# Kernel tuning notes

Hardware: AMD Instinct MI355X
Metric: run time of the kernel (lower is better)

The kernel has to match this reference:

```python
import jax, jax.numpy as jnp
import numpy as np

B, C_FEAT, C_CODE, H, W = 32, 768, 70, 28, 28
FS = 11
NEG = 5
POS_INTRA_SHIFT = 0.18
POS_INTER_SHIFT = 0.12
NEG_INTER_SHIFT = 0.46


def _norm(t):
    # F.normalize(t, dim=1, eps=1e-10)
    n = jnp.sqrt(jnp.sum(t * t, axis=1, keepdims=True))
    return t / jnp.maximum(n, 1e-10)


def _grid_sample(t, coords):
    # torch: F.grid_sample(t, coords.permute(0,2,1,3), padding_mode='border', align_corners=True)
    grid = jnp.transpose(coords, (0, 2, 1, 3))  # [N, Hg, Wg, 2], last dim = (x, y)
    N, C, Hi, Wi = t.shape
    # align_corners=True unnormalize, then border-clip the continuous coordinate
    x = jnp.clip((grid[..., 0] + 1.0) * 0.5 * (Wi - 1), 0.0, Wi - 1.0)
    y = jnp.clip((grid[..., 1] + 1.0) * 0.5 * (Hi - 1), 0.0, Hi - 1.0)
    x0 = jnp.floor(x)
    y0 = jnp.floor(y)
    wx = (x - x0)[:, None]  # broadcast over channel dim
    wy = (y - y0)[:, None]
    x0i = x0.astype(jnp.int32)
    y0i = y0.astype(jnp.int32)
    x1i = jnp.minimum(x0i + 1, Wi - 1)
    y1i = jnp.minimum(y0i + 1, Hi - 1)
    gather = jax.vmap(lambda img, yi, xi: img[:, yi, xi])  # [C,Hg,Wg] per batch elem
    v00 = gather(t, y0i, x0i)
    v01 = gather(t, y0i, x1i)
    v10 = gather(t, y1i, x0i)
    v11 = gather(t, y1i, x1i)
    return (v00 * (1.0 - wx) * (1.0 - wy) + v01 * wx * (1.0 - wy)
            + v10 * (1.0 - wx) * wy + v11 * wx * wy)


def _helper(f1, f2, c1, c2, shift):
    # fd under torch.no_grad -> stop_gradient
    fd = jnp.einsum('nchw,ncij->nhwij', _norm(f1), _norm(f2))
    old_mean = fd.mean()  # pointwise=True branch
    fd = fd - fd.mean(axis=(3, 4), keepdims=True)
    fd = jax.lax.stop_gradient(fd - fd.mean() + old_mean)
    cd = jnp.einsum('nchw,ncij->nhwij', _norm(c1), _norm(c2))
    # zero_clamp=True -> min_val=0.0; stabalize=True -> clamp max 0.8
    loss = -jnp.clip(cd, 0.0, 0.8) * (fd - shift)
    return loss, cd


def _forward(orig_feats, orig_feats_pos, orig_code, orig_code_pos,
             depth_aug_feats, depth_aug_feats_pos, coords1, coords2, perms):
    c1 = coords1 * 2.0 - 1.0
    c2 = coords2 * 2.0 - 1.0
    feats = _grid_sample(orig_feats, c1)
    code = _grid_sample(orig_code, c1)
    feats_pos = _grid_sample(orig_feats_pos, c2)
    code_pos = _grid_sample(orig_code_pos, c2)
    daf = _grid_sample(depth_aug_feats, c1)
    _ = _grid_sample(depth_aug_feats_pos, c2)  # computed (as in torch) but unused

    pos_intra_loss, pos_intra_cd = _helper(daf, daf, code, code, POS_INTRA_SHIFT)
    pos_inter_loss, pos_inter_cd = _helper(feats, feats_pos, code, code_pos, POS_INTER_SHIFT)

    neg_losses, neg_cds = [], []
    for i in range(perms.shape[0]):  # fixed small neg_samples loop
        p = perms[i]
        feats_neg = _grid_sample(orig_feats[p], c2)
        code_neg = _grid_sample(orig_code[p], c2)
        l, cd = _helper(feats, feats_neg, code, code_neg, NEG_INTER_SHIFT)
        neg_losses.append(l)
        neg_cds.append(cd)
    neg_inter_loss = jnp.concatenate(neg_losses, axis=0)
    neg_inter_cd = jnp.concatenate(neg_cds, axis=0)
    return (pos_intra_loss.mean(), pos_intra_cd,
            pos_inter_loss.mean(), pos_inter_cd,
            neg_inter_loss, neg_inter_cd)


def setup_inputs() -> dict:
    key = jax.random.key(0)
    ks = jax.random.split(key, 10)
    rng = np.random.default_rng(0)
    perms = []
    for _ in range(NEG):  # super_perm: derangement-ish permutation
        p = rng.permutation(B)
        p = np.where(p == np.arange(B), p + 1, p) % B
        perms.append(p)
    return {
        'orig_feats': jax.random.normal(ks[0], (B, C_FEAT, H, W), jnp.float32),
        'orig_feats_pos': jax.random.normal(ks[1], (B, C_FEAT, H, W), jnp.float32),
        'orig_salience': jnp.zeros((B, H, W), jnp.float32),
        'orig_salience_pos': jnp.zeros((B, H, W), jnp.float32),
        'orig_code': jax.random.normal(ks[2], (B, C_CODE, H, W), jnp.float32),
        'orig_code_pos': jax.random.normal(ks[3], (B, C_CODE, H, W), jnp.float32),
        'depth_aug_feats': jax.random.normal(ks[4], (B, C_FEAT, H, W), jnp.float32),
        'depth_aug_feats_pos': jax.random.normal(ks[5], (B, C_FEAT, H, W), jnp.float32),
        'coords1': jax.random.uniform(ks[6], (B, FS, FS, 2), jnp.float32),
        'coords2': jax.random.uniform(ks[7], (B, FS, FS, 2), jnp.float32),
        'perms': jnp.asarray(np.stack(perms), dtype=jnp.int32),
    }


def reference(orig_feats, orig_feats_pos, orig_salience, orig_salience_pos,
              orig_code, orig_code_pos, depth_aug_feats, depth_aug_feats_pos,
              coords1, coords2, perms):
    # use_salience=False: salience tensors unused
    return _forward(orig_feats, orig_feats_pos, orig_code, orig_code_pos,
                    depth_aug_feats, depth_aug_feats_pos, coords1, coords2, perms)
```

## Files before the change

### kernel.cpp

```cpp
#include <hip/hip_runtime.h>

#define CF 768
#define CCODE 70
#define NPIX 784
#define P 121
#define NB 32
#define NTOTF 468512.0f

#define OFF_PI_SCALAR 0
#define OFF_PI_CD 1
#define OFF_PO_SCALAR 468513
#define OFF_PO_CD 468514
#define OFF_NEG_LOSS 937026
#define OFF_NEG_CD 3279586

#define WS_BSUMS 0
#define WS_ADDT 768
#define WS_INVF 1024
#define WS_INVC 33792
#define WS_FRAG_FLOAT 62464
#define FEAT_FRAG_SHORTS 98304
#define CODE_FRAG_SHORTS 12288
#define FEATS_TOTAL_SHORTS (8 * 32 * FEAT_FRAG_SHORTS)
#define CODE_BASE_SHORTS FEATS_TOTAL_SHORTS
#define CODE_TOTAL_SHORTS (7 * 32 * CODE_FRAG_SHORTS)
#define WS_NEED2 (WS_FRAG_FLOAT + (FEATS_TOTAL_SHORTS + CODE_TOTAL_SHORTS) / 2)

typedef __attribute__((ext_vector_type(8))) short short8;
typedef __attribute__((ext_vector_type(4))) float f32x4;
typedef unsigned short ushort_t;
typedef unsigned int uint_t;

__device__ __forceinline__ float samp4(const float* __restrict__ img, int c,
                                       const int4 o, const float4 w) {
  const float* p = img + c * NPIX;
  return w.x * p[o.x] + w.y * p[o.y] + w.z * p[o.z] + w.w * p[o.w];
}

__device__ __forceinline__ void mkcoord(const float* cp, int4* o, float4* w) {
  float x = fminf(fmaxf(cp[0] * 27.f, 0.f), 27.f);
  float y = fminf(fmaxf(cp[1] * 27.f, 0.f), 27.f);
  float x0f = floorf(x), y0f = floorf(y);
  int x0 = (int)x0f, y0 = (int)y0f;
  int x1 = min(x0 + 1, 27), y1 = min(y0 + 1, 27);
  float wx = x - x0f, wy = y - y0f;
  *o = make_int4(y0 * 28 + x0, y0 * 28 + x1, y1 * 28 + x0, y1 * 28 + x1);
  *w = make_float4((1.f - wx) * (1.f - wy), wx * (1.f - wy),
                   (1.f - wx) * wy, wx * wy);
}

__device__ __forceinline__ void mkcoord2(const float* cp, int2* o, float4* w) {
  float x = fminf(fmaxf(cp[0] * 27.f, 0.f), 27.f);
  float y = fminf(fmaxf(cp[1] * 27.f, 0.f), 27.f);
  float x0f = floorf(x), y0f = floorf(y);
  int x0 = (int)x0f, y0 = (int)y0f;
  int y1 = min(y0 + 1, 27);
  float wx = x - x0f, wy = y - y0f;
  bool sh = (x0 >= 27);
  int xb = sh ? 26 : x0;
  float wa0 = sh ? 0.f : (1.f - wx) * (1.f - wy);
  float wa1 = sh ? (1.f - wy) : wx * (1.f - wy);
  float wb0 = sh ? 0.f : (1.f - wx) * wy;
  float wb1 = sh ? wy : wx * wy;
  *o = make_int2(y0 * 28 + xb, y1 * 28 + xb);
  *w = make_float4(wa0, wa1, wb0, wb1);
}

__device__ __forceinline__ ushort_t f2bf(float x) {
  uint_t u = __float_as_uint(x);
  u += 0x7fffu + ((u >> 16) & 1u);
  return (ushort_t)(u >> 16);
}

__device__ __forceinline__ float bflo(uint_t u) {
  return __uint_as_float(u << 16);
}
__device__ __forceinline__ float bfhi(uint_t u) {
  return __uint_as_float(u & 0xffff0000u);
}

__global__ __launch_bounds__(256) void presample_bal(
    const float* __restrict__ OF, const float* __restrict__ OFP,
    const float* __restrict__ OC, const float* __restrict__ OCP,
    const float* __restrict__ DAF,
    const float* __restrict__ CO1, const float* __restrict__ CO2,
    const int* __restrict__ PERMS, float* __restrict__ ws) {
  ushort_t* frags = (ushort_t*)(ws + WS_FRAG_FLOAT);
  __shared__ float planes[8 * NPIX];
  __shared__ int sh_slot[16], sh_n[16], sh_cb[16];
  __shared__ int sh_ncs;
  const int job = (int)(((long long)blockIdx.x * 1013) % 2560);
  const int tid = threadIdx.x;

  int tensor, m, g0, G;
  if (job < 1536) { tensor = 0; m = job / 48; g0 = (job - m * 48) * 2; G = 2; }
  else if (job < 1920) { int j = job - 1536; tensor = 1; m = j / 12; g0 = (j - m * 12) * 8; G = 8; }
  else if (job < 2304) { int j = job - 1920; tensor = 2; m = j / 12; g0 = (j - m * 12) * 8; G = 8; }
  else if (job < 2496) { int j = job - 2304; tensor = 3; m = j / 6; g0 = (j - m * 6) * 2; G = 2; }
  else { int j = job - 2496; tensor = 4; m = j / 2; g0 = (j - m * 2) * 6; G = 6; }

  const float* src;
  int nch;
  bool feat;
  if (tensor == 0) { src = OF + (size_t)m * CF * NPIX; nch = CF; feat = true; }
  else if (tensor == 1) { src = DAF + (size_t)m * CF * NPIX; nch = CF; feat = true; }
  else if (tensor == 2) { src = OFP + (size_t)m * CF * NPIX; nch = CF; feat = true; }
  else if (tensor == 3) { src = OC + (size_t)m * CCODE * NPIX; nch = CCODE; feat = false; }
  else { src = OCP + (size_t)m * CCODE * NPIX; nch = CCODE; feat = false; }

  if (tid == 0) {
    int cnt = 0;
    if (tensor == 0) {
      sh_slot[0] = 1; sh_n[0] = m; sh_cb[0] = 0; cnt = 1;
      for (int i = 0; i < 5; ++i)
        for (int k = 0; k < NB; ++k)
          if (PERMS[i * NB + k] == m) {
            sh_slot[cnt] = 3 + i; sh_n[cnt] = k; sh_cb[cnt] = 1; ++cnt;
          }
    } else if (tensor == 1) { sh_slot[0] = 0; sh_n[0] = m; sh_cb[0] = 0; cnt = 1; }
    else if (tensor == 2) { sh_slot[0] = 2; sh_n[0] = m; sh_cb[0] = 1; cnt = 1; }
    else if (tensor == 3) {
      sh_slot[0] = 0; sh_n[0] = m; sh_cb[0] = 0; cnt = 1;
      for (int i = 0; i < 5; ++i)
        for (int k = 0; k < NB; ++k)
          if (PERMS[i * NB + k] == m) {
            sh_slot[cnt] = 2 + i; sh_n[cnt] = k; sh_cb[cnt] = 1; ++cnt;
          }
    } else { sh_slot[0] = 1; sh_n[0] = m; sh_cb[0] = 1; cnt = 1; }
    sh_ncs = cnt;
  }

  float4 buf0, buf1, buf2, buf3, buf4, buf5, buf6;
#define LOAD_OCT(OCT)                                                        \
  {                                                                          \
    const int c0_ = (OCT) * 8;                                               \
    int valid_ = nch - c0_;                                                  \
    valid_ = valid_ > 8 ? 8 : (valid_ < 0 ? 0 : valid_);                     \
    const int lim4_ = valid_ * (NPIX / 4);                                   \
    const float4* sc_ = (const float4*)(src + (size_t)c0_ * NPIX);           \
    int e_;                                                                  \
    e_ = tid;          buf0 = (e_ < lim4_) ? sc_[e_] : make_float4(0,0,0,0); \
    e_ = tid + 256;    buf1 = (e_ < lim4_) ? sc_[e_] : make_float4(0,0,0,0); \
    e_ = tid + 512;    buf2 = (e_ < lim4_) ? sc_[e_] : make_float4(0,0,0,0); \
    e_ = tid + 768;    buf3 = (e_ < lim4_) ? sc_[e_] : make_float4(0,0,0,0); \
    e_ = tid + 1024;   buf4 = (e_ < lim4_) ? sc_[e_] : make_float4(0,0,0,0); \
    e_ = tid + 1280;   buf5 = (e_ < lim4_) ? sc_[e_] : make_float4(0,0,0,0); \
    e_ = tid + 1536;                                                         \
    buf6 = (e_ < 1568 && e_ < lim4_) ? sc_[e_] : make_float4(0,0,0,0);       \
  }

  LOAD_OCT(g0);

  for (int g = 0; g < G; ++g) {
    const int o = g0 + g;
    __syncthreads();
    {
      float4* pl4 = (float4*)planes;
      int e;
      e = tid;        pl4[e] = buf0;
      e = tid + 256;  pl4[e] = buf1;
      e = tid + 512;  pl4[e] = buf2;
      e = tid + 768;  pl4[e] = buf3;
      e = tid + 1024; pl4[e] = buf4;
      e = tid + 1280; pl4[e] = buf5;
      e = tid + 1536; if (e < 1568) pl4[e] = buf6;
    }
    __syncthreads();
    if (g + 1 < G) LOAD_OCT(g0 + g + 1);

    const int kp = o >> 2, lg = o & 3;
    const int total = sh_ncs * 128;
    for (int s = tid; s < total; s += 256) {
      const int cs = s >> 7, pt = s & 127;
      const int slot = sh_slot[cs], n = sh_n[cs];
      const float* cb = sh_cb[cs] ? CO2 : CO1;
      float v[8];
      if (pt < P) {
        int gi = pt / 11, gj = pt - gi * 11;
        int2 o2;
        float4 w4;
        mkcoord2(cb + (((n * 11 + gj) * 11 + gi) << 1), &o2, &w4);
#pragma unroll
        for (int i = 0; i < 8; ++i) {
          const float* pl = planes + i * NPIX;
          v[i] = w4.x * pl[o2.x] + w4.y * pl[o2.x + 1] + w4.z * pl[o2.y] +
                 w4.w * pl[o2.y + 1];
        }
      } else {
#pragma unroll
        for (int i = 0; i < 8; ++i) v[i] = 0.f;
      }
      uint4 q;
      q.x = (uint_t)f2bf(v[0]) | ((uint_t)f2bf(v[1]) << 16);
      q.y = (uint_t)f2bf(v[2]) | ((uint_t)f2bf(v[3]) << 16);
      q.z = (uint_t)f2bf(v[4]) | ((uint_t)f2bf(v[5]) << 16);
      q.w = (uint_t)f2bf(v[6]) | ((uint_t)f2bf(v[7]) << 16);
      size_t fragbase = feat ? (size_t)(slot * 32 + n) * FEAT_FRAG_SHORTS
                             : CODE_BASE_SHORTS + (size_t)(slot * 32 + n) * CODE_FRAG_SHORTS;
      *(uint4*)(frags + fragbase +
                ((size_t)((kp * 8 + (pt >> 4)) * 64 + lg * 16 + (pt & 15)) << 3)) = q;
    }
  }
#undef LOAD_OCT
}

__global__ __launch_bounds__(128) void norms_kernel(float* __restrict__ ws) {
  const ushort_t* frags = (const ushort_t*)(ws + WS_FRAG_FLOAT);
  const int b = blockIdx.x, p = threadIdx.x;
  float s = 0.f;
  if (b < 256) {
    const int slot = b >> 5, n = b & 31;
    const uint4* F = (const uint4*)(frags + (size_t)(slot * 32 + n) * FEAT_FRAG_SHORTS);
    for (int kp = 0; kp < 24; ++kp) {
#pragma unroll
      for (int lg = 0; lg < 4; ++lg) {
        uint4 q = F[(kp * 8 + (p >> 4)) * 64 + lg * 16 + (p & 15)];
        float a;
        a = bflo(q.x); s = fmaf(a, a, s); a = bfhi(q.x); s = fmaf(a, a, s);
        a = bflo(q.y); s = fmaf(a, a, s); a = bfhi(q.y); s = fmaf(a, a, s);
        a = bflo(q.z); s = fmaf(a, a, s); a = bfhi(q.z); s = fmaf(a, a, s);
        a = bflo(q.w); s = fmaf(a, a, s); a = bfhi(q.w); s = fmaf(a, a, s);
      }
    }
    ws[WS_INVF + (slot * 32 + n) * 128 + p] = 1.f / fmaxf(sqrtf(s), 1e-10f);
  } else {
    const int b2 = b - 256;
    const int slot = b2 >> 5, n = b2 & 31;
    const uint4* F = (const uint4*)(frags + CODE_BASE_SHORTS +
                                    (size_t)(slot * 32 + n) * CODE_FRAG_SHORTS);
#pragma unroll
    for (int kp = 0; kp < 3; ++kp) {
#pragma unroll
      for (int lg = 0; lg < 4; ++lg) {
        uint4 q = F[(kp * 8 + (p >> 4)) * 64 + lg * 16 + (p & 15)];
        float a;
        a = bflo(q.x); s = fmaf(a, a, s); a = bfhi(q.x); s = fmaf(a, a, s);
        a = bflo(q.y); s = fmaf(a, a, s); a = bfhi(q.y); s = fmaf(a, a, s);
        a = bflo(q.z); s = fmaf(a, a, s); a = bfhi(q.z); s = fmaf(a, a, s);
        a = bflo(q.w); s = fmaf(a, a, s); a = bfhi(q.w); s = fmaf(a, a, s);
      }
    }
    ws[WS_INVC + (slot * 32 + n) * 128 + p] = 1.f / fmaxf(sqrtf(s), 1e-10f);
  }
}

__global__ __launch_bounds__(256) void gram_mfma(float* __restrict__ ws,
                                                 float* __restrict__ out) {
  const ushort_t* frags = (const ushort_t*)(ws + WS_FRAG_FLOAT);
  const int bid = blockIdx.x, pair = bid >> 5, n = bid & 31;
  const int tid = threadIdx.x, wave = tid >> 6, lane = tid & 63;
  __shared__ float invAf[128], invBf[128], invAc[128], invBc[128];
  __shared__ float red[4][3];
  const int afslot = (pair == 0) ? 0 : 1;
  const int bfslot = (pair == 0) ? 0 : (pair == 1 ? 2 : 3 + (pair - 2));
  const int bcslot = (pair == 0) ? 0 : (pair == 1 ? 1 : 2 + (pair - 2));
  if (tid < 128) {
    invAf[tid] = ws[WS_INVF + (afslot * 32 + n) * 128 + tid];
    invBf[tid] = ws[WS_INVF + (bfslot * 32 + n) * 128 + tid];
    invAc[tid] = ws[WS_INVC + (0 * 32 + n) * 128 + tid];
    invBc[tid] = ws[WS_INVC + (bcslot * 32 + n) * 128 + tid];
  }
  __syncthreads();

  const short8* Af = (const short8*)(frags + (size_t)(afslot * 32 + n) * FEAT_FRAG_SHORTS);
  const short8* Bf = (const short8*)(frags + (size_t)(bfslot * 32 + n) * FEAT_FRAG_SHORTS);

  f32x4 acc[2][8];
#pragma unroll
  for (int j = 0; j < 2; ++j)
#pragma unroll
    for (int t = 0; t < 8; ++t) acc[j][t] = (f32x4){0.f, 0.f, 0.f, 0.f};

#pragma unroll 2
  for (int kp = 0; kp < 24; ++kp) {
    short8 a0 = Af[(kp * 8 + 2 * wave) * 64 + lane];
    short8 a1 = Af[(kp * 8 + 2 * wave + 1) * 64 + lane];
    short8 bv[8];
#pragma unroll
    for (int t = 0; t < 8; ++t) bv[t] = Bf[(kp * 8 + t) * 64 + lane];
#pragma unroll
    for (int t = 0; t < 8; ++t) {
      acc[0][t] = __builtin_amdgcn_mfma_f32_16x16x32_bf16(a0, bv[t], acc[0][t], 0, 0, 0);
      acc[1][t] = __builtin_amdgcn_mfma_f32_16x16x32_bf16(a1, bv[t], acc[1][t], 0, 0, 0);
    }
  }

  const int lane4 = (lane >> 4) << 2;
  const int cl15 = lane & 15;
  float sfd = 0.f;
#pragma unroll
  for (int j = 0; j < 2; ++j) {
    const int rb = (2 * wave + j) * 16 + lane4;
    const float ivr0 = invAf[rb], ivr1 = invAf[rb + 1], ivr2 = invAf[rb + 2],
                ivr3 = invAf[rb + 3];
    float rs0 = 0.f, rs1 = 0.f, rs2 = 0.f, rs3 = 0.f;
#pragma unroll
    for (int t = 0; t < 8; ++t) {
      const float ivc = invBf[t * 16 + cl15];
      float v0 = acc[j][t].x * ivr0 * ivc;
      float v1 = acc[j][t].y * ivr1 * ivc;
      float v2 = acc[j][t].z * ivr2 * ivc;
      float v3 = acc[j][t].w * ivr3 * ivc;
      acc[j][t].x = v0; acc[j][t].y = v1; acc[j][t].z = v2; acc[j][t].w = v3;
      rs0 += v0; rs1 += v1; rs2 += v2; rs3 += v3;
    }
    sfd += rs0 + rs1 + rs2 + rs3;
    rs0 += __shfl_xor(rs0, 1); rs0 += __shfl_xor(rs0, 2);
    rs0 += __shfl_xor(rs0, 4); rs0 += __shfl_xor(rs0, 8);
    rs1 += __shfl_xor(rs1, 1); rs1 += __shfl_xor(rs1, 2);
    rs1 += __shfl_xor(rs1, 4); rs1 += __shfl_xor(rs1, 8);
    rs2 += __shfl_xor(rs2, 1); rs2 += __shfl_xor(rs2, 2);
    rs2 += __shfl_xor(rs2, 4); rs2 += __shfl_xor(rs2, 8);
    rs3 += __shfl_xor(rs3, 1); rs3 += __shfl_xor(rs3, 2);
    rs3 += __shfl_xor(rs3, 4); rs3 += __shfl_xor(rs3, 8);
    const float rm0 = rs0 * (1.f / 121.f), rm1 = rs1 * (1.f / 121.f);
    const float rm2 = rs2 * (1.f / 121.f), rm3 = rs3 * (1.f / 121.f);
#pragma unroll
    for (int t = 0; t < 8; ++t) {
      acc[j][t].x -= rm0; acc[j][t].y -= rm1; acc[j][t].z -= rm2; acc[j][t].w -= rm3;
    }
  }

  int cd_base, loss_base = 0;
  if (pair == 0) cd_base = OFF_PI_CD + n * 14641;
  else if (pair == 1) cd_base = OFF_PO_CD + n * 14641;
  else {
    int t0 = ((pair - 2) * NB + n) * 14641;
    cd_base = OFF_NEG_CD + t0;
    loss_base = OFF_NEG_LOSS + t0;
  }

  if (pair >= 2) {
#pragma unroll
    for (int j = 0; j < 2; ++j) {
      const int rb = (2 * wave + j) * 16 + lane4;
      if (rb < P) {
#pragma unroll
        for (int t = 0; t < 8; ++t) {
          const int c = t * 16 + cl15;
          if (c < P) {
            float* o = out + loss_base + rb * P + c;
            o[0] = acc[j][t].x;
            if (rb + 1 < P) o[P] = acc[j][t].y;
            if (rb + 2 < P) o[2 * P] = acc[j][t].z;
            if (rb + 3 < P) o[3 * P] = acc[j][t].w;
          }
        }
      }
    }
  }

  const short8* Ac = (const short8*)(frags + CODE_BASE_SHORTS + (size_t)n * CODE_FRAG_SHORTS);
  const short8* Bc = (const short8*)(frags + CODE_BASE_SHORTS + (size_t)(bcslot * 32 + n) * CODE_FRAG_SHORTS);
  f32x4 cacc[2][8];
#pragma unroll
  for (int j = 0; j < 2; ++j)
#pragma unroll
    for (int t = 0; t < 8; ++t) cacc[j][t] = (f32x4){0.f, 0.f, 0.f, 0.f};
#pragma unroll
  for (int kp = 0; kp < 3; ++kp) {
    short8 a0 = Ac[(kp * 8 + 2 * wave) * 64 + lane];
    short8 a1 = Ac[(kp * 8 + 2 * wave + 1) * 64 + lane];
    short8 bv[8];
#pragma unroll
    for (int t = 0; t < 8; ++t) bv[t] = Bc[(kp * 8 + t) * 64 + lane];
#pragma unroll
    for (int t = 0; t < 8; ++t) {
      cacc[0][t] = __builtin_amdgcn_mfma_f32_16x16x32_bf16(a0, bv[t], cacc[0][t], 0, 0, 0);
      cacc[1][t] = __builtin_amdgcn_mfma_f32_16x16x32_bf16(a1, bv[t], cacc[1][t], 0, 0, 0);
    }
  }

  float s1 = 0.f, s2 = 0.f;
#pragma unroll
  for (int j = 0; j < 2; ++j) {
    const int rb = (2 * wave + j) * 16 + lane4;
    const float ivr0 = invAc[rb], ivr1 = invAc[rb + 1], ivr2 = invAc[rb + 2],
                ivr3 = invAc[rb + 3];
#pragma unroll
    for (int t = 0; t < 8; ++t) {
      const int c = t * 16 + cl15;
      const float ivc = invBc[c];
      float c0v = cacc[j][t].x * ivr0 * ivc;
      float c1v = cacc[j][t].y * ivr1 * ivc;
      float c2v = cacc[j][t].z * ivr2 * ivc;
      float c3v = cacc[j][t].w * ivr3 * ivc;
      if (c < P && rb < P) {
        float* o = out + cd_base + rb * P + c;
        o[0] = c0v;
        if (rb + 1 < P) o[P] = c1v;
        if (rb + 2 < P) o[2 * P] = c2v;
        if (rb + 3 < P) o[3 * P] = c3v;
      }
      if (pair < 2) {
        float cl0 = fminf(fmaxf(c0v, 0.f), 0.8f);
        float cl1 = fminf(fmaxf(c1v, 0.f), 0.8f);
        float cl2 = fminf(fmaxf(c2v, 0.f), 0.8f);
        float cl3 = fminf(fmaxf(c3v, 0.f), 0.8f);
        s1 = fmaf(cl0, acc[j][t].x, s1);
        s1 = fmaf(cl1, acc[j][t].y, s1);
        s1 = fmaf(cl2, acc[j][t].z, s1);
        s1 = fmaf(cl3, acc[j][t].w, s1);
        s2 += cl0 + cl1 + cl2 + cl3;
      }
    }
  }

#pragma unroll
  for (int m = 1; m < 64; m <<= 1) {
    sfd += __shfl_xor(sfd, m);
    s1 += __shfl_xor(s1, m);
    s2 += __shfl_xor(s2, m);
  }
  if ((tid & 63) == 0) { red[wave][0] = sfd; red[wave][1] = s1; red[wave][2] = s2; }
  __syncthreads();
  if (tid == 0) {
    float a = 0.f, b2 = 0.f, c2 = 0.f;
    for (int w = 0; w < 4; ++w) { a += red[w][0]; b2 += red[w][1]; c2 += red[w][2]; }
    float* bsums = ws + WS_BSUMS;
    bsums[bid * 3 + 0] = a;
    bsums[bid * 3 + 1] = b2;
    bsums[bid * 3 + 2] = c2;
  }
}

__global__ void loss_finish2(float* __restrict__ ws, float* __restrict__ out) {
  __shared__ float s[7][3];
  const float* bsums = ws + WS_BSUMS;
  float* addterm = ws + WS_ADDT;
  int tid = threadIdx.x;
  if (tid < 21) {
    int pr = tid / 3, k = tid % 3;
    float a = 0.f;
    for (int i = 0; i < 32; ++i) a += bsums[(pr * 32 + i) * 3 + k];
    s[pr][k] = a;
  }
  __syncthreads();
  if (tid == 0) {
    const float invN = 1.f / NTOTF;
    out[OFF_PI_SCALAR] = -(s[0][1] + (s[0][0] * invN - 0.18f) * s[0][2]) * invN;
    out[OFF_PO_SCALAR] = -(s[1][1] + (s[1][0] * invN - 0.12f) * s[1][2]) * invN;
  }
  if (tid >= 1 && tid < 6) addterm[tid - 1] = s[tid + 1][0] / NTOTF - 0.46f;
}

__global__ __launch_bounds__(256) void neg_loss_kernel(
    float* __restrict__ lossr, const float* __restrict__ cdr,
    const float* __restrict__ addterm) {
  __shared__ float at[5];
  if (threadIdx.x < 5) at[threadIdx.x] = addterm[threadIdx.x];
  __syncthreads();
  const int total4 = 5 * 117128;
  float4* l4 = (float4*)lossr;
  const float4* c4 = (const float4*)cdr;
  for (int e = blockIdx.x * 256 + threadIdx.x; e < total4; e += gridDim.x * 256) {
    int k = e / 117128;
    float4 cd = c4[e];
    float4 fv = l4[e];
    float a = at[k];
    float4 r;
    r.x = -fminf(fmaxf(cd.x, 0.f), 0.8f) * (fv.x + a);
    r.y = -fminf(fmaxf(cd.y, 0.f), 0.8f) * (fv.y + a);
    r.z = -fminf(fmaxf(cd.z, 0.f), 0.8f) * (fv.z + a);
    r.w = -fminf(fmaxf(cd.w, 0.f), 0.8f) * (fv.w + a);
    l4[e] = r;
  }
}


__global__ __launch_bounds__(256) void loss_main_fb(
    const float* __restrict__ OF, const float* __restrict__ OFP,
    const float* __restrict__ OC, const float* __restrict__ OCP,
    const float* __restrict__ DAF,
    const float* __restrict__ CO1, const float* __restrict__ CO2,
    const int* __restrict__ PERMS,
    float* __restrict__ out, float* __restrict__ bsums) {
  const int b = blockIdx.x;
  const int pair = b >> 7;
  const int rem = b & 127;
  const int n = rem >> 2;
  const int rg = rem & 3;
  const int row_start = rg * 31;
  const int rcount = min(31, P - row_start);
  const int tid = threadIdx.x;
  const int tx = tid & 15, ty = tid >> 4;

  const float *F1, *F2, *C1, *C2, *CB;
  if (pair == 0) {
    F1 = DAF + (size_t)n * CF * NPIX; F2 = F1;
    C1 = OC + (size_t)n * CCODE * NPIX; C2 = C1;
    CB = CO1;
  } else if (pair == 1) {
    F1 = OF + (size_t)n * CF * NPIX; F2 = OFP + (size_t)n * CF * NPIX;
    C1 = OC + (size_t)n * CCODE * NPIX; C2 = OCP + (size_t)n * CCODE * NPIX;
    CB = CO2;
  } else {
    int n2 = PERMS[(pair - 2) * NB + n];
    F1 = OF + (size_t)n * CF * NPIX; F2 = OF + (size_t)n2 * CF * NPIX;
    C1 = OC + (size_t)n * CCODE * NPIX; C2 = OC + (size_t)n2 * CCODE * NPIX;
    CB = CO2;
  }

  __shared__ int4 Bo[P];
  __shared__ float4 Bw[P];
  __shared__ int4 Ao[32];
  __shared__ float4 Aw[32];
  __shared__ float Abuf[CCODE][32];
  __shared__ float Bbuf[CCODE][128];
  __shared__ float invA[32], invB[128];
  __shared__ float red[4][3];

  if (tid < P) {
    int gi = tid / 11, gj = tid - gi * 11;
    const float* cp = CB + (((n * 11 + gj) * 11 + gi) << 1);
    mkcoord(cp, &Bo[tid], &Bw[tid]);
  } else if (tid >= 128 && tid < 160) {
    int r = tid - 128;
    int q = row_start + r;
    if (q < P) {
      int gi = q / 11, gj = q - gi * 11;
      const float* cp = CO1 + (((n * 11 + gj) * 11 + gi) << 1);
      mkcoord(cp, &Ao[r], &Aw[r]);
    }
  }
  __syncthreads();

  float acc[2][2][4];
#pragma unroll
  for (int kr = 0; kr < 2; ++kr)
#pragma unroll
    for (int m = 0; m < 2; ++m)
#pragma unroll
      for (int u = 0; u < 4; ++u) acc[kr][m][u] = 0.f;
  float ansq = 0.f, bnsq = 0.f;

  for (int ch = 0; ch < 12; ++ch) {
    const int c0 = ch * 64;
    if (ch) __syncthreads();
    for (int e = tid; e < 64 * 128; e += 256) {
      int col = e & 127, cc = e >> 7;
      float v = 0.f;
      if (col < P) v = samp4(F2, c0 + cc, Bo[col], Bw[col]);
      Bbuf[cc][col] = v;
    }
    for (int e = tid; e < 64 * 32; e += 256) {
      int col = e & 31, cc = e >> 5;
      float v = 0.f;
      if (col < rcount) v = samp4(F1, c0 + cc, Ao[col], Aw[col]);
      Abuf[cc][col] = v;
    }
    __syncthreads();
    if (tid < 128) {
      float s = 0.f;
      for (int cc = 0; cc < 64; ++cc) { float v = Bbuf[cc][tid]; s = fmaf(v, v, s); }
      bnsq += s;
    } else if (tid < 160) {
      int r = tid - 128;
      float s = 0.f;
      for (int cc = 0; cc < 64; ++cc) { float v = Abuf[cc][r]; s = fmaf(v, v, s); }
      ansq += s;
    }
    for (int cc = 0; cc < 64; ++cc) {
      const float2 av = *(const float2*)&Abuf[cc][ty * 2];
      const float4 b0 = *(const float4*)&Bbuf[cc][tx * 4];
      const float4 b1 = *(const float4*)&Bbuf[cc][tx * 4 + 64];
      float a[2] = {av.x, av.y};
      float bb[2][4] = {{b0.x, b0.y, b0.z, b0.w}, {b1.x, b1.y, b1.z, b1.w}};
#pragma unroll
      for (int kr = 0; kr < 2; ++kr)
#pragma unroll
        for (int m = 0; m < 2; ++m)
#pragma unroll
          for (int u = 0; u < 4; ++u)
            acc[kr][m][u] = fmaf(a[kr], bb[m][u], acc[kr][m][u]);
    }
  }
  __syncthreads();
  if (tid < 128) invB[tid] = (tid < P) ? 1.f / fmaxf(sqrtf(bnsq), 1e-10f) : 0.f;
  else if (tid < 160) {
    int r = tid - 128;
    invA[r] = (r < rcount) ? 1.f / fmaxf(sqrtf(ansq), 1e-10f) : 0.f;
  }
  __syncthreads();

  float ia[2] = {invA[2 * ty], invA[2 * ty + 1]};
  float ib[2][4];
#pragma unroll
  for (int m = 0; m < 2; ++m)
#pragma unroll
    for (int u = 0; u < 4; ++u) ib[m][u] = invB[m * 64 + tx * 4 + u];

  float fdc[2][2][4];
  float sfd = 0.f;
#pragma unroll
  for (int kr = 0; kr < 2; ++kr) {
    float part = 0.f;
#pragma unroll
    for (int m = 0; m < 2; ++m)
#pragma unroll
      for (int u = 0; u < 4; ++u) {
        float v = acc[kr][m][u] * ia[kr] * ib[m][u];
        fdc[kr][m][u] = v;
        part += v;
      }
    sfd += part;
    float rs = part;
#pragma unroll
    for (int s = 1; s < 16; s <<= 1) rs += __shfl_xor(rs, s, 16);
    float rowm = rs * (1.f / 121.f);
#pragma unroll
    for (int m = 0; m < 2; ++m)
#pragma unroll
      for (int u = 0; u < 4; ++u) fdc[kr][m][u] -= rowm;
  }
  __syncthreads();

  for (int e = tid; e < CCODE * 128; e += 256) {
    int col = e & 127, cc = e >> 7;
    float v = 0.f;
    if (col < P) v = samp4(C2, cc, Bo[col], Bw[col]);
    Bbuf[cc][col] = v;
  }
  for (int e = tid; e < CCODE * 32; e += 256) {
    int col = e & 31, cc = e >> 5;
    float v = 0.f;
    if (col < rcount) v = samp4(C1, cc, Ao[col], Aw[col]);
    Abuf[cc][col] = v;
  }
  __syncthreads();
  if (tid < 128) {
    float s = 0.f;
    for (int cc = 0; cc < CCODE; ++cc) { float v = Bbuf[cc][tid]; s = fmaf(v, v, s); }
    invB[tid] = (tid < P) ? 1.f / fmaxf(sqrtf(s), 1e-10f) : 0.f;
  } else if (tid < 160) {
    int r = tid - 128;
    float s = 0.f;
    for (int cc = 0; cc < CCODE; ++cc) { float v = Abuf[cc][r]; s = fmaf(v, v, s); }
    invA[r] = (r < rcount) ? 1.f / fmaxf(sqrtf(s), 1e-10f) : 0.f;
  }
  float cacc[2][2][4];
#pragma unroll
  for (int kr = 0; kr < 2; ++kr)
#pragma unroll
    for (int m = 0; m < 2; ++m)
#pragma unroll
      for (int u = 0; u < 4; ++u) cacc[kr][m][u] = 0.f;
  for (int cc = 0; cc < CCODE; ++cc) {
    const float2 av = *(const float2*)&Abuf[cc][ty * 2];
    const float4 b0 = *(const float4*)&Bbuf[cc][tx * 4];
    const float4 b1 = *(const float4*)&Bbuf[cc][tx * 4 + 64];
    float a[2] = {av.x, av.y};
    float bb[2][4] = {{b0.x, b0.y, b0.z, b0.w}, {b1.x, b1.y, b1.z, b1.w}};
#pragma unroll
    for (int kr = 0; kr < 2; ++kr)
#pragma unroll
      for (int m = 0; m < 2; ++m)
#pragma unroll
        for (int u = 0; u < 4; ++u)
          cacc[kr][m][u] = fmaf(a[kr], bb[m][u], cacc[kr][m][u]);
  }
  __syncthreads();
  float iac[2] = {invA[2 * ty], invA[2 * ty + 1]};
  float ibc[2][4];
#pragma unroll
  for (int m = 0; m < 2; ++m)
#pragma unroll
    for (int u = 0; u < 4; ++u) ibc[m][u] = invB[m * 64 + tx * 4 + u];

  int cd_base, loss_base = 0;
  if (pair == 0) cd_base = OFF_PI_CD + n * 14641;
  else if (pair == 1) cd_base = OFF_PO_CD + n * 14641;
  else {
    int t = ((pair - 2) * NB + n) * 14641;
    cd_base = OFF_NEG_CD + t;
    loss_base = OFF_NEG_LOSS + t;
  }

  float s1 = 0.f, s2 = 0.f;
#pragma unroll
  for (int kr = 0; kr < 2; ++kr) {
    int r = 2 * ty + kr;
    if (r < rcount) {
      int rglob = row_start + r;
#pragma unroll
      for (int m = 0; m < 2; ++m)
#pragma unroll
        for (int u = 0; u < 4; ++u) {
          int c = m * 64 + tx * 4 + u;
          if (c < P) {
            float cdv = cacc[kr][m][u] * iac[kr] * ibc[m][u];
            int idx = rglob * P + c;
            out[cd_base + idx] = cdv;
            float cl = fminf(fmaxf(cdv, 0.f), 0.8f);
            float fv = fdc[kr][m][u];
            if (pair < 2) { s1 = fmaf(cl, fv, s1); s2 += cl; }
            else out[loss_base + idx] = fv;
          }
        }
    }
  }

#pragma unroll
  for (int s = 1; s < 64; s <<= 1) {
    sfd += __shfl_xor(sfd, s);
    s1 += __shfl_xor(s1, s);
    s2 += __shfl_xor(s2, s);
  }
  int wv = tid >> 6;
  if ((tid & 63) == 0) { red[wv][0] = sfd; red[wv][1] = s1; red[wv][2] = s2; }
  __syncthreads();
  if (tid == 0) {
    float a = 0.f, bb = 0.f, cc = 0.f;
    for (int w = 0; w < 4; ++w) { a += red[w][0]; bb += red[w][1]; cc += red[w][2]; }
    bsums[b * 3 + 0] = a;
    bsums[b * 3 + 1] = bb;
    bsums[b * 3 + 2] = cc;
  }
}

__global__ void loss_finish_fb(const float* __restrict__ bsums,
                               float* __restrict__ out,
                               float* __restrict__ addterm) {
  __shared__ float s[7][3];
  int tid = threadIdx.x;
  if (tid < 21) {
    int pr = tid / 3, k = tid % 3;
    float a = 0.f;
    const float* p = bsums + (pr * 128) * 3 + k;
    for (int i = 0; i < 128; ++i) a += p[i * 3];
    s[pr][k] = a;
  }
  __syncthreads();
  if (tid == 0) {
    const float invN = 1.f / NTOTF;
    out[OFF_PI_SCALAR] = -(s[0][1] + (s[0][0] * invN - 0.18f) * s[0][2]) * invN;
    out[OFF_PO_SCALAR] = -(s[1][1] + (s[1][0] * invN - 0.12f) * s[1][2]) * invN;
  }
  if (tid >= 1 && tid < 6) addterm[tid - 1] = s[tid + 1][0] / NTOTF - 0.46f;
}

__global__ __launch_bounds__(256) void neg_loss_fb(
    float* __restrict__ lossr, const float* __restrict__ cdr,
    const float* __restrict__ addterm) {
  __shared__ float at[5];
  if (threadIdx.x < 5) at[threadIdx.x] = addterm[threadIdx.x];
  __syncthreads();
  const int total = 5 * 468512;
  for (int e = blockIdx.x * 256 + threadIdx.x; e < total; e += gridDim.x * 256) {
    int k = e / 468512;
    float cdv = cdr[e];
    float cl = fminf(fmaxf(cdv, 0.f), 0.8f);
    lossr[e] = -cl * (lossr[e] + at[k]);
  }
}

extern "C" void kernel_launch(void* const* d_in, const int* in_sizes, int n_in,
                              void* d_out, int out_size, void* d_ws,
                              size_t ws_size, hipStream_t stream) {
  const float* OF = (const float*)d_in[0];
  const float* OFP = (const float*)d_in[1];
  const float* OC = (const float*)d_in[4];
  const float* OCP = (const float*)d_in[5];
  const float* DAF = (const float*)d_in[6];
  const float* CO1 = (const float*)d_in[8];
  const float* CO2 = (const float*)d_in[9];
  const int* PERMS = (const int*)d_in[10];
  float* out = (float*)d_out;
  float* ws = (float*)d_ws;

  if (ws_size >= (size_t)WS_NEED2 * sizeof(float)) {
    hipLaunchKernelGGL(presample_bal, dim3(2560), dim3(256), 0, stream,
                       OF, OFP, OC, OCP, DAF, CO1, CO2, PERMS, ws);
    hipLaunchKernelGGL(norms_kernel, dim3(480), dim3(128), 0, stream, ws);
    hipLaunchKernelGGL(gram_mfma, dim3(224), dim3(256), 0, stream, ws, out);
    hipLaunchKernelGGL(loss_finish2, dim3(1), dim3(64), 0, stream, ws, out);
    hipLaunchKernelGGL(neg_loss_kernel, dim3(1024), dim3(256), 0, stream,
                       out + OFF_NEG_LOSS, out + OFF_NEG_CD, ws + WS_ADDT);
  } else {
    float* bsums = ws;
    float* addterm = bsums + 896 * 3;
    hipLaunchKernelGGL(loss_main_fb, dim3(896), dim3(256), 0, stream,
                       OF, OFP, OC, OCP, DAF, CO1, CO2, PERMS, out, bsums);
    hipLaunchKernelGGL(loss_finish_fb, dim3(1), dim3(64), 0, stream,
                       bsums, out, addterm);
    hipLaunchKernelGGL(neg_loss_fb, dim3(2048), dim3(256), 0, stream,
                       out + OFF_NEG_LOSS, out + OFF_NEG_CD, addterm);
  }
}
```

Before: 152.6 us.

## Hoist bilinear coordinate setup out of octet loop and rebalance presample jobs

```diff
diff --git a/kernel.cpp b/kernel.cpp
--- a/kernel.cpp
+++ b/kernel.cpp
@@ -79,7 +79,7 @@
   return __uint_as_float(u & 0xffff0000u);
 }
 
-__global__ __launch_bounds__(256) void presample_bal(
+__global__ __launch_bounds__(256) void presample_hoist(
     const float* __restrict__ OF, const float* __restrict__ OFP,
     const float* __restrict__ OC, const float* __restrict__ OCP,
     const float* __restrict__ DAF,
@@ -89,15 +89,15 @@
   __shared__ float planes[8 * NPIX];
   __shared__ int sh_slot[16], sh_n[16], sh_cb[16];
   __shared__ int sh_ncs;
-  const int job = (int)(((long long)blockIdx.x * 1013) % 2560);
+  const int job = (int)(((long long)blockIdx.x * 405) % 1216);
   const int tid = threadIdx.x;
 
   int tensor, m, g0, G;
-  if (job < 1536) { tensor = 0; m = job / 48; g0 = (job - m * 48) * 2; G = 2; }
-  else if (job < 1920) { int j = job - 1536; tensor = 1; m = j / 12; g0 = (j - m * 12) * 8; G = 8; }
-  else if (job < 2304) { int j = job - 1920; tensor = 2; m = j / 12; g0 = (j - m * 12) * 8; G = 8; }
-  else if (job < 2496) { int j = job - 2304; tensor = 3; m = j / 6; g0 = (j - m * 6) * 2; G = 2; }
-  else { int j = job - 2496; tensor = 4; m = j / 2; g0 = (j - m * 2) * 6; G = 6; }
+  if (job < 384) { tensor = 0; m = job / 12; g0 = (job - m * 12) * 8; G = 8; }
+  else if (job < 768) { int j = job - 384; tensor = 1; m = j / 12; g0 = (j - m * 12) * 8; G = 8; }
+  else if (job < 1152) { int j = job - 768; tensor = 2; m = j / 12; g0 = (j - m * 12) * 8; G = 8; }
+  else if (job < 1184) { tensor = 3; m = job - 1152; g0 = 0; G = 12; }
+  else { tensor = 4; m = job - 1184; g0 = 0; G = 12; }
 
   const float* src;
   int nch;
@@ -150,10 +150,58 @@
   }
 
   LOAD_OCT(g0);
+  __syncthreads();
+
+  const int total = sh_ncs * 128;
+  int2 o_0, o_1, o_2, o_3, o_4, o_5;
+  float4 w_0, w_1, w_2, w_3, w_4, w_5;
+  uint_t b_0 = 0, b_1 = 0, b_2 = 0, b_3 = 0, b_4 = 0, b_5 = 0;
+#define SETUP_SLOT(J, OV, WV, BV)                                            \
+  {                                                                          \
+    const int s_ = tid + (J) * 256;                                          \
+    OV = make_int2(0, 0);                                                    \
+    WV = make_float4(0.f, 0.f, 0.f, 0.f);                                    \
+    if (s_ < total) {                                                        \
+      const int cs_ = s_ >> 7, pt_ = s_ & 127;                               \
+      const int slot_ = sh_slot[cs_], n_ = sh_n[cs_];                        \
+      const float* cb_ = sh_cb[cs_] ? CO2 : CO1;                             \
+      size_t fb_ = feat ? (size_t)(slot_ * 32 + n_) * FEAT_FRAG_SHORTS       \
+                        : CODE_BASE_SHORTS +                                 \
+                              (size_t)(slot_ * 32 + n_) * CODE_FRAG_SHORTS;  \
+      BV = (uint_t)(fb_ + ((size_t)((pt_ >> 4) * 64 + (pt_ & 15)) << 3));    \
+      if (pt_ < P) {                                                         \
+        int gi_ = pt_ / 11, gj_ = pt_ - gi_ * 11;                            \
+        mkcoord2(cb_ + (((n_ * 11 + gj_) * 11 + gi_) << 1), &OV, &WV);       \
+      }                                                                      \
+    }                                                                        \
+  }
+  SETUP_SLOT(0, o_0, w_0, b_0)
+  SETUP_SLOT(1, o_1, w_1, b_1)
+  SETUP_SLOT(2, o_2, w_2, b_2)
+  SETUP_SLOT(3, o_3, w_3, b_3)
+  SETUP_SLOT(4, o_4, w_4, b_4)
+  SETUP_SLOT(5, o_5, w_5, b_5)
+#undef SETUP_SLOT
+
+#define DO_SLOT(J, OV, WV, BV)                                               \
+  if (tid + (J) * 256 < total) {                                             \
+    float v_[8];                                                             \
+    _Pragma("unroll") for (int i_ = 0; i_ < 8; ++i_) {                       \
+      const float* pl_ = planes + i_ * NPIX;                                 \
+      v_[i_] = WV.x * pl_[OV.x] + WV.y * pl_[OV.x + 1] +                     \
+               WV.z * pl_[OV.y] + WV.w * pl_[OV.y + 1];                      \
+    }                                                                        \
+    uint4 q_;                                                                \
+    q_.x = (uint_t)f2bf(v_[0]) | ((uint_t)f2bf(v_[1]) << 16);                \
+    q_.y = (uint_t)f2bf(v_[2]) | ((uint_t)f2bf(v_[3]) << 16);                \
+    q_.z = (uint_t)f2bf(v_[4]) | ((uint_t)f2bf(v_[5]) << 16);                \
+    q_.w = (uint_t)f2bf(v_[6]) | ((uint_t)f2bf(v_[7]) << 16);                \
+    *(uint4*)(frags + BV + octoff) = q_;                                     \
+  }
 
   for (int g = 0; g < G; ++g) {
     const int o = g0 + g;
-    __syncthreads();
+    if (g) __syncthreads();
     {
       float4* pl4 = (float4*)planes;
       int e;
@@ -168,39 +216,15 @@
     __syncthreads();
     if (g + 1 < G) LOAD_OCT(g0 + g + 1);
 
-    const int kp = o >> 2, lg = o & 3;
-    const int total = sh_ncs * 128;
-    for (int s = tid; s < total; s += 256) {
-      const int cs = s >> 7, pt = s & 127;
-      const int slot = sh_slot[cs], n = sh_n[cs];
-      const float* cb = sh_cb[cs] ? CO2 : CO1;
-      float v[8];
-      if (pt < P) {
-        int gi = pt / 11, gj = pt - gi * 11;
-        int2 o2;
-        float4 w4;
-        mkcoord2(cb + (((n * 11 + gj) * 11 + gi) << 1), &o2, &w4);
-#pragma unroll
-        for (int i = 0; i < 8; ++i) {
-          const float* pl = planes + i * NPIX;
-          v[i] = w4.x * pl[o2.x] + w4.y * pl[o2.x + 1] + w4.z * pl[o2.y] +
-                 w4.w * pl[o2.y + 1];
-        }
-      } else {
-#pragma unroll
-        for (int i = 0; i < 8; ++i) v[i] = 0.f;
-      }
-      uint4 q;
-      q.x = (uint_t)f2bf(v[0]) | ((uint_t)f2bf(v[1]) << 16);
-      q.y = (uint_t)f2bf(v[2]) | ((uint_t)f2bf(v[3]) << 16);
-      q.z = (uint_t)f2bf(v[4]) | ((uint_t)f2bf(v[5]) << 16);
-      q.w = (uint_t)f2bf(v[6]) | ((uint_t)f2bf(v[7]) << 16);
-      size_t fragbase = feat ? (size_t)(slot * 32 + n) * FEAT_FRAG_SHORTS
-                             : CODE_BASE_SHORTS + (size_t)(slot * 32 + n) * CODE_FRAG_SHORTS;
-      *(uint4*)(frags + fragbase +
-                ((size_t)((kp * 8 + (pt >> 4)) * 64 + lg * 16 + (pt & 15)) << 3)) = q;
-    }
-  }
+    const uint_t octoff = (uint_t)((o >> 2) * 4096 + (o & 3) * 128);
+    DO_SLOT(0, o_0, w_0, b_0)
+    DO_SLOT(1, o_1, w_1, b_1)
+    DO_SLOT(2, o_2, w_2, b_2)
+    DO_SLOT(3, o_3, w_3, b_3)
+    DO_SLOT(4, o_4, w_4, b_4)
+    DO_SLOT(5, o_5, w_5, b_5)
+  }
+#undef DO_SLOT
 #undef LOAD_OCT
 }
 
@@ -769,7 +793,7 @@
   float* ws = (float*)d_ws;
 
   if (ws_size >= (size_t)WS_NEED2 * sizeof(float)) {
-    hipLaunchKernelGGL(presample_bal, dim3(2560), dim3(256), 0, stream,
+    hipLaunchKernelGGL(presample_hoist, dim3(1216), dim3(256), 0, stream,
                        OF, OFP, OC, OCP, DAF, CO1, CO2, PERMS, ws);
     hipLaunchKernelGGL(norms_kernel, dim3(480), dim3(128), 0, stream, ws);
     hipLaunchKernelGGL(gram_mfma, dim3(224), dim3(256), 0, stream, ws, out);
```

Result: faster. 145.2 us (-4.8%).
